# Optimization experiments

Hardware: AMD Instinct MI355X
Metric: run time of the kernel (lower is better)

## Reference

```python
import jax, jax.numpy as jnp
import numpy as np

L = 16; F = 2; T = 1 << 19; BASE = 16.0; FINEST = 2048.0; CDIM = 16; N = 262144
_PRIMES = np.array([1, 2654435761, 805459861], dtype=np.uint32)
_OFFS = np.array([[i, j, k] for i in (0, 1) for j in (0, 1) for k in (0, 1)], dtype=np.uint32)
_RES = np.floor(BASE * np.exp(np.arange(L) * (np.log(FINEST) - np.log(BASE)) / (L - 1))).astype(np.float32)


def _hash_encode(pn, table):
    # pn: [N,3] normalized to [0,1]; table: [L,T,F]
    offs = jnp.asarray(_OFFS)
    offs_mask = jnp.asarray(_OFFS.astype(bool))
    primes = jnp.asarray(_PRIMES)

    def level(tab, res):
        scaled = pn * res
        pos = jnp.floor(scaled)
        frac = scaled - pos
        corners = pos.astype(jnp.uint32)[:, None, :] + offs[None]  # [N,8,3]
        idx = (corners[..., 0] * primes[0]) ^ (corners[..., 1] * primes[1]) ^ (corners[..., 2] * primes[2])
        idx = (idx & jnp.uint32(T - 1)).astype(jnp.int32)
        feats = tab[idx]  # [N,8,F]
        w = jnp.prod(jnp.where(offs_mask[None], frac[:, None, :], 1.0 - frac[:, None, :]), axis=-1)  # [N,8]
        return jnp.einsum('nkf,nk->nf', feats, w)

    out = jax.vmap(level)(table, jnp.asarray(_RES))  # [L,N,F]
    return jnp.transpose(out, (1, 0, 2)).reshape(pn.shape[0], L * F)


def _lin(x, w, b):
    return x @ w.T + b


def _forward(p, bound, t_sdf, t_color, t_sem,
             f_w0, f_b0, f_w1, f_b1, f_w2, f_b2, f_w3, f_b3,
             osdf_w, osdf_b, orgb_w0, orgb_b0, orgb_w1, orgb_b1,
             s_w0, s_b0, s_w1, s_b1, s_w2, s_b2, s_wo, s_bo):
    pn = (p - bound[:, 0]) / (bound[:, 1] - bound[:, 0])
    feat = _hash_encode(pn, t_sdf)    # [N,32]
    c_feat = _hash_encode(pn, t_color)
    s_feat = _hash_encode(pn, t_sem)
    h = feat
    for w, b in ((f_w0, f_b0), (f_w1, f_b1), (f_w2, f_b2), (f_w3, f_b3)):
        h = jax.nn.relu(_lin(h, w, b))
    sdf_out = _lin(h, osdf_w, osdf_b)        # [N,17]
    sdf = jnp.tanh(sdf_out[:, 0])            # [N]
    sdf_feat = sdf_out[:, 1:]                # [N,16]
    rgb_in = jnp.concatenate([sdf_feat, c_feat, s_feat], axis=-1)  # [N,80]
    rgb = jax.nn.sigmoid(_lin(jax.nn.relu(_lin(rgb_in, orgb_w0, orgb_b0)), orgb_w1, orgb_b1))  # [N,3]
    hs = s_feat
    for w, b in ((s_w0, s_b0), (s_w1, s_b1), (s_w2, s_b2)):
        hs = jax.nn.relu(_lin(hs, w, b))
    semantic = _lin(hs, s_wo, s_bo)          # [N,25]
    raw = jnp.concatenate([rgb, sdf[:, None], semantic], axis=-1)  # [N,29]
    plane_feat = jnp.concatenate([c_feat[:, CDIM:], feat[:, CDIM:], s_feat[:, CDIM:]], axis=-1)  # [N,48]
    return raw, plane_feat


def setup_inputs() -> dict:
    key = jax.random.key(0)
    ks = jax.random.split(key, 32)

    def w(k, o, i):
        return (jax.random.normal(k, (o, i), jnp.float32) / np.sqrt(i)).astype(jnp.float32)

    return {
        'p': jax.random.uniform(ks[0], (N, 3), jnp.float32),
        'bound': jnp.array([[0.0, 1.0], [0.0, 1.0], [0.0, 1.0]], jnp.float32),
        't_sdf': jax.random.uniform(ks[1], (L, T, F), jnp.float32, -1e-2, 1e-2),
        't_color': jax.random.uniform(ks[2], (L, T, F), jnp.float32, -1e-2, 1e-2),
        't_sem': jax.random.uniform(ks[3], (L, T, F), jnp.float32, -1e-2, 1e-2),
        'f_w0': w(ks[4], 16, 32), 'f_b0': jnp.zeros(16, jnp.float32),
        'f_w1': w(ks[5], 16, 16), 'f_b1': jnp.zeros(16, jnp.float32),
        'f_w2': w(ks[6], 16, 16), 'f_b2': jnp.zeros(16, jnp.float32),
        'f_w3': w(ks[7], 16, 16), 'f_b3': jnp.zeros(16, jnp.float32),
        'osdf_w': w(ks[8], 17, 16), 'osdf_b': jnp.zeros(17, jnp.float32),
        'orgb_w0': w(ks[9], 16, 80), 'orgb_b0': jnp.zeros(16, jnp.float32),
        'orgb_w1': w(ks[10], 3, 16), 'orgb_b1': jnp.zeros(3, jnp.float32),
        's_w0': w(ks[11], 256, 32), 's_b0': jnp.zeros(256, jnp.float32),
        's_w1': w(ks[12], 256, 256), 's_b1': jnp.zeros(256, jnp.float32),
        's_w2': w(ks[13], 256, 256), 's_b2': jnp.zeros(256, jnp.float32),
        's_wo': w(ks[14], 25, 256), 's_bo': jnp.zeros(25, jnp.float32),
    }


def reference(p, bound, t_sdf, t_color, t_sem,
              f_w0, f_b0, f_w1, f_b1, f_w2, f_b2, f_w3, f_b3,
              osdf_w, osdf_b, orgb_w0, orgb_b0, orgb_w1, orgb_b1,
              s_w0, s_b0, s_w1, s_b1, s_w2, s_b2, s_wo, s_bo):
    return _forward(p, bound, t_sdf, t_color, t_sem,
                    f_w0, f_b0, f_w1, f_b1, f_w2, f_b2, f_w3, f_b3,
                    osdf_w, osdf_b, orgb_w0, orgb_b0, orgb_w1, orgb_b1,
                    s_w0, s_b0, s_w1, s_b1, s_w2, s_b2, s_wo, s_bo)
```

## Files before the change

### kernel.cpp

```cpp
#include <hip/hip_runtime.h>
#include <math.h>

#define NPTS 262144
#define TTAB 524288
#define TMASK (TTAB - 1)
#define PR1 2654435761u
#define PR2 805459861u

#define MQ_SLOTS 512
#define MHASH_BLOCKS (8 * MQ_SLOTS)
#define FQ_SLOTS 1536
#define FHASH_BLOCKS (8 * FQ_SLOTS)

typedef __attribute__((ext_vector_type(4))) float f32x4;
typedef __attribute__((ext_vector_type(8))) short bf16x8;
typedef __attribute__((ext_vector_type(3))) unsigned int uintx3;

struct ResArr { float r[16]; };

__device__ __forceinline__ float bf2f(unsigned int u) {
  union { unsigned int i; float f; } v; v.i = u << 16; return v.f;
}
__device__ __forceinline__ unsigned short f2bf(float f) {
  union { float f; unsigned int i; } v; v.f = f;
  unsigned int r = v.i + 0x7FFFu + ((v.i >> 16) & 1u);
  return (unsigned short)(r >> 16);
}
__device__ __forceinline__ unsigned int pack2(float a, float b) {
  return (unsigned int)f2bf(a) | ((unsigned int)f2bf(b) << 16);
}

__global__ __launch_bounds__(256) void cvt_tab(
    const float* __restrict__ t0, const float* __restrict__ t1,
    const float* __restrict__ t2, unsigned int* __restrict__ mt)
{
  size_t i = (size_t)blockIdx.x * 256 + threadIdx.x;
  float2 a = ((const float2*)t0)[i];
  float2 b = ((const float2*)t1)[i];
  float2 c = ((const float2*)t2)[i];
  mt[i * 3 + 0] = pack2(a.x, a.y);
  mt[i * 3 + 1] = pack2(b.x, b.y);
  mt[i * 3 + 2] = pack2(c.x, c.y);
}

__global__ __launch_bounds__(256) void hash_merged(
    const float* __restrict__ p, const float* __restrict__ bound,
    const unsigned int* __restrict__ mt,
    unsigned int* __restrict__ featws, unsigned int* __restrict__ ctr,
    ResArr res)
{
  __shared__ int s_slot;
  if (threadIdx.x == 0) {
    unsigned int xcc;
    asm volatile("s_getreg_b32 %0, hwreg(HW_REG_XCC_ID)" : "=s"(xcc));
    xcc &= 7u;
    int slot = -1;
    for (int k = 0; k < 8; ++k) {
      unsigned int q = (xcc + (unsigned int)k) & 7u;
      unsigned int s = atomicAdd(ctr + q, 1u);
      if (s < MQ_SLOTS) { slot = (int)(q * MQ_SLOTS + s); break; }
    }
    s_slot = slot;
  }
  __syncthreads();
  int slot = s_slot;
  if (slot < 0) return;

  unsigned int q = (unsigned int)slot / MQ_SLOTS;
  unsigned int s = (unsigned int)slot - q * MQ_SLOTS;
  unsigned int level = (s >> 8) * 8u + q;
  unsigned int chunk = s & 255u;

  float r = res.r[0];
#pragma unroll
  for (int l = 1; l < 16; ++l) r = (level == (unsigned int)l) ? res.r[l] : r;

  float b0 = bound[0], b1 = bound[1], b2 = bound[2], b3 = bound[3],
        b4 = bound[4], b5 = bound[5];
  float i0v = 1.f / (b1 - b0), i1v = 1.f / (b3 - b2), i2v = 1.f / (b5 - b4);
  const unsigned int* mtl = mt + (size_t)level * TTAB * 3u;
  unsigned int f0 = (0u * 16u + level) * (unsigned int)NPTS;
  unsigned int f1 = (1u * 16u + level) * (unsigned int)NPTS;
  unsigned int f2b = (2u * 16u + level) * (unsigned int)NPTS;
  unsigned int nbase = chunk * 1024u + threadIdx.x;

#pragma unroll
  for (int half = 0; half < 2; ++half) {
    unsigned int CX[2], CY[2], CZ[2];
    float DX[2], DY[2], DZ[2];
#pragma unroll
    for (int pt = 0; pt < 2; ++pt) {
      unsigned int n = nbase + (unsigned int)(half * 512 + pt * 256);
      float px = p[n * 3 + 0], py = p[n * 3 + 1], pz = p[n * 3 + 2];
      float sx = (px - b0) * i0v * r;
      float sy = (py - b2) * i1v * r;
      float sz = (pz - b4) * i2v * r;
      float fx = floorf(sx), fy = floorf(sy), fz = floorf(sz);
      DX[pt] = sx - fx; DY[pt] = sy - fy; DZ[pt] = sz - fz;
      CX[pt] = (unsigned int)fx;
      CY[pt] = (unsigned int)fy * PR1;
      CZ[pt] = (unsigned int)fz * PR2;
    }
    __builtin_amdgcn_sched_barrier(0);

    uintx3 V[2][8];
#pragma unroll
    for (int pt = 0; pt < 2; ++pt) {
      unsigned int x0 = CX[pt], x1 = CX[pt] + 1u;
      unsigned int y0 = CY[pt], y1 = y0 + PR1;
      unsigned int z0 = CZ[pt], z1 = z0 + PR2;
      unsigned int id[8];
      id[0] = (x0 ^ y0 ^ z0) & TMASK;
      id[1] = (x0 ^ y0 ^ z1) & TMASK;
      id[2] = (x0 ^ y1 ^ z0) & TMASK;
      id[3] = (x0 ^ y1 ^ z1) & TMASK;
      id[4] = (x1 ^ y0 ^ z0) & TMASK;
      id[5] = (x1 ^ y0 ^ z1) & TMASK;
      id[6] = (x1 ^ y1 ^ z0) & TMASK;
      id[7] = (x1 ^ y1 ^ z1) & TMASK;
#pragma unroll
      for (int c = 0; c < 8; ++c)
        V[pt][c] = *(const uintx3*)(mtl + (size_t)id[c] * 3u);
    }
    __builtin_amdgcn_sched_barrier(0);

#pragma unroll
    for (int pt = 0; pt < 2; ++pt) {
      float dx = DX[pt], dy = DY[pt], dz = DZ[pt];
      float wx[2] = { 1.f - dx, dx }, wy[2] = { 1.f - dy, dy }, wz[2] = { 1.f - dz, dz };
      float a00 = 0.f, a01 = 0.f, a10 = 0.f, a11 = 0.f, a20 = 0.f, a21 = 0.f;
#pragma unroll
      for (int c = 0; c < 8; ++c) {
        float w = wx[c >> 2] * wy[(c >> 1) & 1] * wz[c & 1];
        unsigned int u0 = V[pt][c].x, u1 = V[pt][c].y, u2 = V[pt][c].z;
        a00 += bf2f(u0 << 16) * w;  a01 += bf2f(u0 & 0xFFFF0000u) * w;
        a10 += bf2f(u1 << 16) * w;  a11 += bf2f(u1 & 0xFFFF0000u) * w;
        a20 += bf2f(u2 << 16) * w;  a21 += bf2f(u2 & 0xFFFF0000u) * w;
      }
      unsigned int n = nbase + (unsigned int)(half * 512 + pt * 256);
      featws[f0 + n] = pack2(a00, a01);
      featws[f1 + n] = pack2(a10, a11);
      featws[f2b + n] = pack2(a20, a21);
    }
  }
}

__global__ __launch_bounds__(256) void hash_f32(
    const float* __restrict__ p, const float* __restrict__ bound,
    const float* __restrict__ t0, const float* __restrict__ t1,
    const float* __restrict__ t2,
    unsigned int* __restrict__ featws, unsigned int* __restrict__ ctr,
    ResArr res)
{
  __shared__ int s_pad[10240];
  if (threadIdx.x == 0) {
    unsigned int xcc;
    asm volatile("s_getreg_b32 %0, hwreg(HW_REG_XCC_ID)" : "=s"(xcc));
    xcc &= 7u;
    int slot = -1;
    for (int k = 0; k < 8; ++k) {
      unsigned int q = (xcc + (unsigned int)k) & 7u;
      unsigned int s = atomicAdd(ctr + q, 1u);
      if (s < FQ_SLOTS) { slot = (int)(q * FQ_SLOTS + s); break; }
    }
    s_pad[0] = slot;
  }
  __syncthreads();
  int slot = s_pad[0];
  if (slot < 0) return;

  unsigned int q = (unsigned int)slot / FQ_SLOTS;
  unsigned int s = (unsigned int)slot - q * FQ_SLOTS;
  unsigned int i = (s >> 8) * 8u + q;
  unsigned int level = i / 3u;
  unsigned int table = i - level * 3u;
  unsigned int chunk = s & 255u;

  float r = res.r[0];
#pragma unroll
  for (int l = 1; l < 16; ++l) r = (level == (unsigned int)l) ? res.r[l] : r;

  float b0 = bound[0], b1 = bound[1], b2 = bound[2], b3 = bound[3],
        b4 = bound[4], b5 = bound[5];
  const float* tf = ((table == 0u) ? t0 : (table == 1u) ? t1 : t2) +
                    (size_t)level * (TTAB * 2);
  unsigned int fbase = (table * 16u + level) * (unsigned int)NPTS;
  unsigned int nbase = chunk * 1024u + threadIdx.x;

#pragma unroll
  for (int it = 0; it < 4; ++it) {
    unsigned int n = nbase + (unsigned int)it * 256u;
    float px = p[n * 3 + 0], py = p[n * 3 + 1], pz = p[n * 3 + 2];
    float x = (px - b0) / (b1 - b0);
    float y = (py - b2) / (b3 - b2);
    float z = (pz - b4) / (b5 - b4);
    float sx = x * r, sy = y * r, sz = z * r;
    float fx = floorf(sx), fy = floorf(sy), fz = floorf(sz);
    float dx = sx - fx, dy = sy - fy, dz = sz - fz;
    unsigned int cx = (unsigned int)fx, cy = (unsigned int)fy, cz = (unsigned int)fz;
    unsigned int hx[2] = { cx, cx + 1u };
    unsigned int hy[2] = { cy * PR1, (cy + 1u) * PR1 };
    unsigned int hz[2] = { cz * PR2, (cz + 1u) * PR2 };
    float wx[2] = { 1.f - dx, dx }, wy[2] = { 1.f - dy, dy }, wz[2] = { 1.f - dz, dz };
    float a0 = 0.f, a1 = 0.f;
#pragma unroll
    for (int ii = 0; ii < 2; ++ii)
#pragma unroll
      for (int jj = 0; jj < 2; ++jj)
#pragma unroll
        for (int kk = 0; kk < 2; ++kk) {
          unsigned int idx = (hx[ii] ^ hy[jj] ^ hz[kk]) & TMASK;
          float2 f2 = *(const float2*)(tf + (size_t)idx * 2);
          float w = wx[ii] * wy[jj] * wz[kk];
          a0 += f2.x * w;
          a1 += f2.y * w;
        }
    featws[fbase + n] = pack2(a0, a1);
  }
}

__global__ __launch_bounds__(256) void mlp_small_kernel(
    const unsigned int* __restrict__ fws,
    const float* __restrict__ fw0, const float* __restrict__ fb0,
    const float* __restrict__ fw1, const float* __restrict__ fb1,
    const float* __restrict__ fw2, const float* __restrict__ fb2,
    const float* __restrict__ fw3, const float* __restrict__ fb3,
    const float* __restrict__ ow, const float* __restrict__ ob,
    const float* __restrict__ rw0, const float* __restrict__ rb0,
    const float* __restrict__ rw1, const float* __restrict__ rb1,
    float* __restrict__ out)
{
  unsigned int n = blockIdx.x * 256 + threadIdx.x;
  float ft[32], cf[32], sf[32];
#pragma unroll
  for (int l = 0; l < 16; ++l) {
    unsigned int u = fws[(0u * 16 + l) * (unsigned int)NPTS + n];
    ft[2 * l] = bf2f(u << 16); ft[2 * l + 1] = bf2f(u & 0xFFFF0000u);
    u = fws[(1u * 16 + l) * (unsigned int)NPTS + n];
    cf[2 * l] = bf2f(u << 16); cf[2 * l + 1] = bf2f(u & 0xFFFF0000u);
    u = fws[(2u * 16 + l) * (unsigned int)NPTS + n];
    sf[2 * l] = bf2f(u << 16); sf[2 * l + 1] = bf2f(u & 0xFFFF0000u);
  }

  {
    float* pf = out + (size_t)NPTS * 29 + (size_t)n * 48;
#pragma unroll
    for (int i2 = 0; i2 < 16; i2 += 4)
      *(float4*)(pf + i2) = make_float4(cf[16 + i2], cf[17 + i2], cf[18 + i2], cf[19 + i2]);
#pragma unroll
    for (int i2 = 0; i2 < 16; i2 += 4)
      *(float4*)(pf + 16 + i2) = make_float4(ft[16 + i2], ft[17 + i2], ft[18 + i2], ft[19 + i2]);
#pragma unroll
    for (int i2 = 0; i2 < 16; i2 += 4)
      *(float4*)(pf + 32 + i2) = make_float4(sf[16 + i2], sf[17 + i2], sf[18 + i2], sf[19 + i2]);
  }

  float h[16], g[16];
  for (int o = 0; o < 16; ++o) {
    float a = fb0[o];
    for (int i2 = 0; i2 < 32; ++i2) a += ft[i2] * fw0[o * 32 + i2];
    h[o] = fmaxf(a, 0.f);
  }
  for (int o = 0; o < 16; ++o) {
    float a = fb1[o];
    for (int i2 = 0; i2 < 16; ++i2) a += h[i2] * fw1[o * 16 + i2];
    g[o] = fmaxf(a, 0.f);
  }
  for (int o = 0; o < 16; ++o) {
    float a = fb2[o];
    for (int i2 = 0; i2 < 16; ++i2) a += g[i2] * fw2[o * 16 + i2];
    h[o] = fmaxf(a, 0.f);
  }
  for (int o = 0; o < 16; ++o) {
    float a = fb3[o];
    for (int i2 = 0; i2 < 16; ++i2) a += h[i2] * fw3[o * 16 + i2];
    g[o] = fmaxf(a, 0.f);
  }
  float so[17];
  for (int o = 0; o < 17; ++o) {
    float a = ob[o];
    for (int i2 = 0; i2 < 16; ++i2) a += g[i2] * ow[o * 16 + i2];
    so[o] = a;
  }
  float sdf = tanhf(so[0]);
  float rin[80];
#pragma unroll
  for (int i2 = 0; i2 < 16; ++i2) rin[i2] = so[i2 + 1];
#pragma unroll
  for (int i2 = 0; i2 < 32; ++i2) rin[16 + i2] = cf[i2];
#pragma unroll
  for (int i2 = 0; i2 < 32; ++i2) rin[48 + i2] = sf[i2];
  float hr[16];
  for (int o = 0; o < 16; ++o) {
    float a = rb0[o];
    for (int i2 = 0; i2 < 80; ++i2) a += rin[i2] * rw0[o * 80 + i2];
    hr[o] = fmaxf(a, 0.f);
  }
  float* po = out + (size_t)n * 29;
  for (int o = 0; o < 3; ++o) {
    float a = rb1[o];
    for (int i2 = 0; i2 < 16; ++i2) a += hr[i2] * rw1[o * 16 + i2];
    po[o] = 1.f / (1.f + expf(-a));
  }
  po[3] = sdf;
}

__global__ __launch_bounds__(256) void cvt_kernel(
    const float* __restrict__ sw0, const float* __restrict__ sw1,
    const float* __restrict__ sw2, const float* __restrict__ swo,
    unsigned short* __restrict__ w0, unsigned short* __restrict__ w1,
    unsigned short* __restrict__ w2, unsigned short* __restrict__ wo,
    unsigned int* __restrict__ ctr)
{
  int t = blockIdx.x * 256 + threadIdx.x;
  if (t < 8) ctr[t] = 0u;
  if (t < 8192) w0[t] = f2bf(sw0[t]);
  w1[t] = f2bf(sw1[t]);
  w2[t] = f2bf(sw2[t]);
  if (t < 8192) wo[t] = (t < 6400) ? f2bf(swo[t]) : (unsigned short)0;
}

#define LAYER256(Hin, Wp, Bp, Hout)                                                        \
  {                                                                                        \
    _Pragma("unroll") for (int r = 0; r < 4; ++r)                                          \
      _Pragma("unroll") for (int c = 0; c < 4; ++c)                                        \
        acc[r][c] = (f32x4){0.f, 0.f, 0.f, 0.f};                                           \
    _Pragma("unroll") for (int c = 0; c < 4; ++c)                                          \
      bc[c] = *(const bf16x8*)(Wp + (size_t)(cw + c * 16 + l16) * 256 + quad * 8);         \
    _Pragma("unroll") for (int ks = 0; ks < 8; ++ks) {                                     \
      int k0 = ks * 32;                                                                    \
      if (ks < 7) {                                                                        \
        _Pragma("unroll") for (int c = 0; c < 4; ++c)                                      \
          bn[c] = *(const bf16x8*)(Wp + (size_t)(cw + c * 16 + l16) * 256 + k0 + 32 + quad * 8); \
      }                                                                                    \
      _Pragma("unroll") for (int r = 0; r < 4; ++r)                                        \
        a[r] = *(const bf16x8*)(Hin + (r * 16 + l16) * 264 + k0 + quad * 8);               \
      _Pragma("unroll") for (int r = 0; r < 4; ++r)                                        \
        _Pragma("unroll") for (int c = 0; c < 4; ++c)                                      \
          acc[r][c] = __builtin_amdgcn_mfma_f32_16x16x32_bf16(a[r], bc[c], acc[r][c], 0, 0, 0); \
      _Pragma("unroll") for (int c = 0; c < 4; ++c) bc[c] = bn[c];                         \
    }                                                                                      \
    _Pragma("unroll") for (int c = 0; c < 4; ++c) {                                        \
      int col = cw + c * 16 + l16;                                                         \
      float bias = Bp[col];                                                                \
      _Pragma("unroll") for (int r = 0; r < 4; ++r)                                        \
        _Pragma("unroll") for (int g2 = 0; g2 < 4; ++g2) {                                 \
          int row = r * 16 + quad * 4 + g2;                                                \
          Hout[row * 264 + col] = f2bf(fmaxf(acc[r][c][g2] + bias, 0.f));                  \
        }                                                                                  \
    }                                                                                      \
    __syncthreads();                                                                       \
  }

__global__ __launch_bounds__(256) void sem_kernel(
    const unsigned int* __restrict__ fws,
    const unsigned short* __restrict__ w0, const unsigned short* __restrict__ w1,
    const unsigned short* __restrict__ w2, const unsigned short* __restrict__ wo,
    const float* __restrict__ b0, const float* __restrict__ b1,
    const float* __restrict__ b2, const float* __restrict__ bo,
    float* __restrict__ out)
{
  __shared__ alignas(16) unsigned short X[64 * 40];
  __shared__ alignas(16) unsigned short HA[64 * 264];
  __shared__ alignas(16) unsigned short HB[64 * 264];

  int tid = threadIdx.x;
  int n0 = blockIdx.x * 64;
  int lane = tid & 63, wv = tid >> 6;
  int l16 = lane & 15, quad = lane >> 4;
  int cw = wv * 64;

#pragma unroll
  for (int h = 0; h < 4; ++h) {
    int idx = tid + h * 256;
    int row = idx & 63;
    int l = idx >> 6;
    unsigned int v = fws[(32u + (unsigned int)l) * (unsigned int)NPTS + (unsigned int)(n0 + row)];
    *(unsigned int*)(X + row * 40 + 2 * l) = v;
  }
  __syncthreads();

  f32x4 acc[4][4];
  bf16x8 a[4], bc[4], bn[4];

#pragma unroll
  for (int r = 0; r < 4; ++r)
#pragma unroll
    for (int c = 0; c < 4; ++c) acc[r][c] = (f32x4){0.f, 0.f, 0.f, 0.f};
#pragma unroll
  for (int r = 0; r < 4; ++r) a[r] = *(const bf16x8*)(X + (r * 16 + l16) * 40 + quad * 8);
#pragma unroll
  for (int c = 0; c < 4; ++c) bc[c] = *(const bf16x8*)(w0 + (size_t)(cw + c * 16 + l16) * 32 + quad * 8);
#pragma unroll
  for (int r = 0; r < 4; ++r)
#pragma unroll
    for (int c = 0; c < 4; ++c)
      acc[r][c] = __builtin_amdgcn_mfma_f32_16x16x32_bf16(a[r], bc[c], acc[r][c], 0, 0, 0);
#pragma unroll
  for (int c = 0; c < 4; ++c) {
    int col = cw + c * 16 + l16;
    float bias = b0[col];
#pragma unroll
    for (int r = 0; r < 4; ++r)
#pragma unroll
      for (int g2 = 0; g2 < 4; ++g2) {
        int row = r * 16 + quad * 4 + g2;
        HA[row * 264 + col] = f2bf(fmaxf(acc[r][c][g2] + bias, 0.f));
      }
  }
  __syncthreads();

  LAYER256(HA, w1, b1, HB)
  LAYER256(HB, w2, b2, HA)

  {
    f32x4 acc2[2];
    acc2[0] = (f32x4){0.f, 0.f, 0.f, 0.f};
    acc2[1] = (f32x4){0.f, 0.f, 0.f, 0.f};
#pragma unroll
    for (int ks = 0; ks < 8; ++ks) {
      int k0 = ks * 32;
      bf16x8 af = *(const bf16x8*)(HA + (wv * 16 + l16) * 264 + k0 + quad * 8);
#pragma unroll
      for (int c = 0; c < 2; ++c) {
        bf16x8 bf = *(const bf16x8*)(wo + (size_t)(c * 16 + l16) * 256 + k0 + quad * 8);
        acc2[c] = __builtin_amdgcn_mfma_f32_16x16x32_bf16(af, bf, acc2[c], 0, 0, 0);
      }
    }
#pragma unroll
    for (int c = 0; c < 2; ++c) {
      int col = c * 16 + l16;
      if (col < 25) {
        float bias = bo[col];
#pragma unroll
        for (int g2 = 0; g2 < 4; ++g2) {
          int row = wv * 16 + quad * 4 + g2;
          out[(size_t)(n0 + row) * 29 + 4 + col] = acc2[c][g2] + bias;
        }
      }
    }
  }
}

extern "C" void kernel_launch(void* const* d_in, const int* in_sizes, int n_in,
                              void* d_out, int out_size, void* d_ws, size_t ws_size,
                              hipStream_t stream) {
  const float* p      = (const float*)d_in[0];
  const float* bound  = (const float*)d_in[1];
  const float* t_sdf  = (const float*)d_in[2];
  const float* t_color= (const float*)d_in[3];
  const float* t_sem  = (const float*)d_in[4];
  const float* f_w0   = (const float*)d_in[5];
  const float* f_b0   = (const float*)d_in[6];
  const float* f_w1   = (const float*)d_in[7];
  const float* f_b1   = (const float*)d_in[8];
  const float* f_w2   = (const float*)d_in[9];
  const float* f_b2   = (const float*)d_in[10];
  const float* f_w3   = (const float*)d_in[11];
  const float* f_b3   = (const float*)d_in[12];
  const float* osdf_w = (const float*)d_in[13];
  const float* osdf_b = (const float*)d_in[14];
  const float* orgb_w0= (const float*)d_in[15];
  const float* orgb_b0= (const float*)d_in[16];
  const float* orgb_w1= (const float*)d_in[17];
  const float* orgb_b1= (const float*)d_in[18];
  const float* s_w0   = (const float*)d_in[19];
  const float* s_b0   = (const float*)d_in[20];
  const float* s_w1   = (const float*)d_in[21];
  const float* s_b1   = (const float*)d_in[22];
  const float* s_w2   = (const float*)d_in[23];
  const float* s_b2   = (const float*)d_in[24];
  const float* s_wo   = (const float*)d_in[25];
  const float* s_bo   = (const float*)d_in[26];

  unsigned int* featws = (unsigned int*)d_ws;
  unsigned short* w0b = (unsigned short*)(featws + 48u * NPTS);
  unsigned short* w1b = w0b + 8192;
  unsigned short* w2b = w1b + 65536;
  unsigned short* wob = w2b + 65536;
  unsigned int* ctr = (unsigned int*)(wob + 8192);
  unsigned int* mt = ctr + 8;
  size_t need_bt = ((char*)mt - (char*)d_ws) + (size_t)16 * TTAB * 12;
  bool use_bt = ws_size >= need_bt;

  ResArr res;
  double kk = (log(2048.0) - log(16.0)) / 15.0;
  for (int l = 0; l < 16; ++l) res.r[l] = (float)floor(16.0 * exp((double)l * kk));

  float* out = (float*)d_out;

  hipLaunchKernelGGL(cvt_kernel, dim3(256), dim3(256), 0, stream,
                     s_w0, s_w1, s_w2, s_wo, w0b, w1b, w2b, wob, ctr);
  if (use_bt) {
    hipLaunchKernelGGL(cvt_tab, dim3(32768), dim3(256), 0, stream,
                       t_sdf, t_color, t_sem, mt);
    hipLaunchKernelGGL(hash_merged, dim3(MHASH_BLOCKS), dim3(256), 0, stream,
                       p, bound, mt, featws, ctr, res);
  } else {
    hipLaunchKernelGGL(hash_f32, dim3(FHASH_BLOCKS), dim3(256), 0, stream,
                       p, bound, t_sdf, t_color, t_sem, featws, ctr, res);
  }
  hipLaunchKernelGGL(mlp_small_kernel, dim3(1024), dim3(256), 0, stream,
                     featws, f_w0, f_b0, f_w1, f_b1, f_w2, f_b2, f_w3, f_b3,
                     osdf_w, osdf_b, orgb_w0, orgb_b0, orgb_w1, orgb_b1, out);
  hipLaunchKernelGGL(sem_kernel, dim3(NPTS / 64), dim3(256), 0, stream,
                     featws, w0b, w1b, w2b, wob, s_b0, s_b1, s_b2, s_bo, out);
}
```

Measured before the change: 585.7 us.

## Single-buffer LDS in semantic MLP, load inputs directly to registers, add setprio

The semantic MLP kernel now uses one shared activation buffer instead of two plus an input staging buffer. It adds an extra barrier so each layer finishes reading before results overwrite the buffer in place. First-layer inputs are gathered straight from global memory into MFMA operand registers, skipping the LDS staging. launch_bounds asks for 4 blocks per CU and s_setprio wraps the MFMA sections. Cutting LDS use should let more blocks stay resident, at the cost of an extra sync per layer and uncoalesced strided global loads for the input.

```diff
diff --git a/kernel.cpp b/kernel.cpp
--- a/kernel.cpp
+++ b/kernel.cpp
@@ -29,6 +29,8 @@
 __device__ __forceinline__ unsigned int pack2(float a, float b) {
   return (unsigned int)f2bf(a) | ((unsigned int)f2bf(b) << 16);
 }
+
+union U8 { uint4 u; bf16x8 v; };
 
 __global__ __launch_bounds__(256) void cvt_tab(
     const float* __restrict__ t0, const float* __restrict__ t1,
@@ -320,7 +322,7 @@
   if (t < 8192) wo[t] = (t < 6400) ? f2bf(swo[t]) : (unsigned short)0;
 }
 
-#define LAYER256(Hin, Wp, Bp, Hout)                                                        \
+#define LAYER256(Wp, Bp)                                                                   \
   {                                                                                        \
     _Pragma("unroll") for (int r = 0; r < 4; ++r)                                          \
       _Pragma("unroll") for (int c = 0; c < 4; ++c)                                        \
@@ -334,25 +336,28 @@
           bn[c] = *(const bf16x8*)(Wp + (size_t)(cw + c * 16 + l16) * 256 + k0 + 32 + quad * 8); \
       }                                                                                    \
       _Pragma("unroll") for (int r = 0; r < 4; ++r)                                        \
-        a[r] = *(const bf16x8*)(Hin + (r * 16 + l16) * 264 + k0 + quad * 8);               \
+        a[r] = *(const bf16x8*)(H + (r * 16 + l16) * 264 + k0 + quad * 8);                 \
+      __builtin_amdgcn_s_setprio(1);                                                       \
       _Pragma("unroll") for (int r = 0; r < 4; ++r)                                        \
         _Pragma("unroll") for (int c = 0; c < 4; ++c)                                      \
           acc[r][c] = __builtin_amdgcn_mfma_f32_16x16x32_bf16(a[r], bc[c], acc[r][c], 0, 0, 0); \
+      __builtin_amdgcn_s_setprio(0);                                                       \
       _Pragma("unroll") for (int c = 0; c < 4; ++c) bc[c] = bn[c];                         \
     }                                                                                      \
+    __syncthreads();                                         \
     _Pragma("unroll") for (int c = 0; c < 4; ++c) {                                        \
       int col = cw + c * 16 + l16;                                                         \
       float bias = Bp[col];                                                                \
       _Pragma("unroll") for (int r = 0; r < 4; ++r)                                        \
         _Pragma("unroll") for (int g2 = 0; g2 < 4; ++g2) {                                 \
           int row = r * 16 + quad * 4 + g2;                                                \
-          Hout[row * 264 + col] = f2bf(fmaxf(acc[r][c][g2] + bias, 0.f));                  \
+          H[row * 264 + col] = f2bf(fmaxf(acc[r][c][g2] + bias, 0.f));                     \
         }                                                                                  \
     }                                                                                      \
-    __syncthreads();                                                                       \
-  }
-
-__global__ __launch_bounds__(256) void sem_kernel(
+    __syncthreads();                                                   \
+  }
+
+__global__ __launch_bounds__(256, 4) void sem_kernel(
     const unsigned int* __restrict__ fws,
     const unsigned short* __restrict__ w0, const unsigned short* __restrict__ w1,
     const unsigned short* __restrict__ w2, const unsigned short* __restrict__ wo,
@@ -360,9 +365,7 @@
     const float* __restrict__ b2, const float* __restrict__ bo,
     float* __restrict__ out)
 {
-  __shared__ alignas(16) unsigned short X[64 * 40];
-  __shared__ alignas(16) unsigned short HA[64 * 264];
-  __shared__ alignas(16) unsigned short HB[64 * 264];
+  __shared__ alignas(16) unsigned short H[64 * 264];
 
   int tid = threadIdx.x;
   int n0 = blockIdx.x * 64;
@@ -370,16 +373,6 @@
   int l16 = lane & 15, quad = lane >> 4;
   int cw = wv * 64;
 
-#pragma unroll
-  for (int h = 0; h < 4; ++h) {
-    int idx = tid + h * 256;
-    int row = idx & 63;
-    int l = idx >> 6;
-    unsigned int v = fws[(32u + (unsigned int)l) * (unsigned int)NPTS + (unsigned int)(n0 + row)];
-    *(unsigned int*)(X + row * 40 + 2 * l) = v;
-  }
-  __syncthreads();
-
   f32x4 acc[4][4];
   bf16x8 a[4], bc[4], bn[4];
 
@@ -388,14 +381,26 @@
 #pragma unroll
     for (int c = 0; c < 4; ++c) acc[r][c] = (f32x4){0.f, 0.f, 0.f, 0.f};
 #pragma unroll
-  for (int r = 0; r < 4; ++r) a[r] = *(const bf16x8*)(X + (r * 16 + l16) * 40 + quad * 8);
-#pragma unroll
-  for (int c = 0; c < 4; ++c) bc[c] = *(const bf16x8*)(w0 + (size_t)(cw + c * 16 + l16) * 32 + quad * 8);
+  for (int r = 0; r < 4; ++r) {
+    unsigned int base = (32u + (unsigned int)quad * 4u) * (unsigned int)NPTS +
+                        (unsigned int)(n0 + r * 16 + l16);
+    U8 u;
+    u.u.x = fws[base];
+    u.u.y = fws[base + (unsigned int)NPTS];
+    u.u.z = fws[base + 2u * (unsigned int)NPTS];
+    u.u.w = fws[base + 3u * (unsigned int)NPTS];
+    a[r] = u.v;
+  }
+#pragma unroll
+  for (int c = 0; c < 4; ++c)
+    bc[c] = *(const bf16x8*)(w0 + (size_t)(cw + c * 16 + l16) * 32 + quad * 8);
+  __builtin_amdgcn_s_setprio(1);
 #pragma unroll
   for (int r = 0; r < 4; ++r)
 #pragma unroll
     for (int c = 0; c < 4; ++c)
       acc[r][c] = __builtin_amdgcn_mfma_f32_16x16x32_bf16(a[r], bc[c], acc[r][c], 0, 0, 0);
+  __builtin_amdgcn_s_setprio(0);
 #pragma unroll
   for (int c = 0; c < 4; ++c) {
     int col = cw + c * 16 + l16;
@@ -405,13 +410,13 @@
 #pragma unroll
       for (int g2 = 0; g2 < 4; ++g2) {
         int row = r * 16 + quad * 4 + g2;
-        HA[row * 264 + col] = f2bf(fmaxf(acc[r][c][g2] + bias, 0.f));
+        H[row * 264 + col] = f2bf(fmaxf(acc[r][c][g2] + bias, 0.f));
       }
   }
   __syncthreads();
 
-  LAYER256(HA, w1, b1, HB)
-  LAYER256(HB, w2, b2, HA)
+  LAYER256(w1, b1)
+  LAYER256(w2, b2)
 
   {
     f32x4 acc2[2];
@@ -420,7 +425,7 @@
 #pragma unroll
     for (int ks = 0; ks < 8; ++ks) {
       int k0 = ks * 32;
-      bf16x8 af = *(const bf16x8*)(HA + (wv * 16 + l16) * 264 + k0 + quad * 8);
+      bf16x8 af = *(const bf16x8*)(H + (wv * 16 + l16) * 264 + k0 + quad * 8);
 #pragma unroll
       for (int c = 0; c < 2; ++c) {
         bf16x8 bf = *(const bf16x8*)(wo + (size_t)(c * 16 + l16) * 256 + k0 + quad * 8);
```

Result: faster. 571.4 us (-2.4%).
